# Kernel optimization log

Measured on AMD Instinct MI355X. Metric: run time of the kernel, lower is better.

Reference implementation:

```python
import jax, jax.numpy as jnp
import numpy as np

DIM = 768
HEADS = 12
HEAD_DIM = DIM // HEADS
EPS = 1e-5


def layernorm(x, gamma, beta):
    mu = jnp.mean(x, axis=-1, keepdims=True)
    var = jnp.var(x, axis=-1, keepdims=True)
    return (x - mu) * jax.lax.rsqrt(var + EPS) * gamma + beta


def setup_inputs() -> dict:
    key = jax.random.key(0)
    ks = jax.random.split(key, 9)
    B, N, C = 4, 2048, DIM
    s_in = 1.0 / np.sqrt(C)
    return {
        "x": jax.random.normal(ks[0], (B, N, C), dtype=jnp.float32),
        "qkv_w": jax.random.normal(ks[1], (3 * C, C), dtype=jnp.float32) * s_in,
        "qkv_b": jnp.zeros((3 * C,), dtype=jnp.float32),
        "proj_w": jax.random.normal(ks[2], (C, C), dtype=jnp.float32) * s_in,
        "proj_b": jnp.zeros((C,), dtype=jnp.float32),
        "q_gamma": jnp.ones((HEAD_DIM,), dtype=jnp.float32),
        "q_beta": jnp.zeros((HEAD_DIM,), dtype=jnp.float32),
        "k_gamma": jnp.ones((HEAD_DIM,), dtype=jnp.float32),
        "k_beta": jnp.zeros((HEAD_DIM,), dtype=jnp.float32),
    }


def reference(x, qkv_w, qkv_b, proj_w, proj_b, q_gamma, q_beta, k_gamma, k_beta):
    B, N, C = x.shape
    H, Dh = HEADS, C // HEADS
    scale = Dh ** (-0.5)
    # qkv projection: [B,N,3C] -> [3,B,H,N,Dh]
    qkv = (x @ qkv_w.T + qkv_b).reshape(B, N, 3, H, Dh).transpose(2, 0, 3, 1, 4)
    q, k, v = qkv[0], qkv[1], qkv[2]
    q = layernorm(q, q_gamma, q_beta)
    k = layernorm(k, k_gamma, k_beta)
    # explicit full score matrix [B,H,N,N] as in the original module
    attn = jnp.einsum("bhqd,bhkd->bhqk", q, k) * scale
    attn = jax.nn.softmax(attn, axis=-1)
    out = jnp.einsum("bhqk,bhkd->bhqd", attn, v)  # [B,H,N,Dh]
    out = out.transpose(0, 2, 1, 3).reshape(B, N, C)
    return out @ proj_w.T + proj_b
```

## Files before the change

### kernel.cpp

```cpp
#include <hip/hip_runtime.h>
#include <hip/hip_bf16.h>
#include <cstdint>
#include <cstddef>

#define BB 4
#define SEQ 2048
#define CD 768
#define NH 12
#define DH 64
#define MROWS (BB*SEQ)
#define NQKV (3*CD)

typedef float f32x4 __attribute__((ext_vector_type(4)));
typedef float f32x16 __attribute__((ext_vector_type(16)));
typedef short bf16x8 __attribute__((ext_vector_type(8)));

static __device__ __forceinline__ unsigned short f2bf(float f) {
  union { float f; unsigned int u; } cv; cv.f = f;
  unsigned int u = cv.u;
  unsigned int r = (u + 0x7FFFu + ((u >> 16) & 1u)) >> 16;
  return (unsigned short)r;
}

static __device__ __forceinline__ float fexp2(float x) {
#if __has_builtin(__builtin_amdgcn_exp2f)
  return __builtin_amdgcn_exp2f(x);
#else
  float r; asm("v_exp_f32 %0, %1" : "=v"(r) : "v"(x)); return r;
#endif
}

#define GAS __attribute__((address_space(1)))
#define LAS __attribute__((address_space(3)))
static __device__ __forceinline__ void gl2lds16(const void* g, void* l) {
  __builtin_amdgcn_global_load_lds((const GAS void*)g, (LAS void*)l, 16, 0, 0);
}

#define MFMA(a, b, c) __builtin_amdgcn_mfma_f32_16x16x32_bf16((a), (b), (c), 0, 0, 0)
#define MFMA32(a, b, c) __builtin_amdgcn_mfma_f32_32x32x16_bf16((a), (b), (c), 0, 0, 0)
#define PACKBF(dst, x, y) asm("v_cvt_pk_bf16_f32 %0, %1, %2" : "=v"(dst) : "v"(x), "v"(y))
#define SWAP32(a, b) asm("v_permlane32_swap_b32 %0, %1" : "+v"(a), "+v"(b))

#define QSC 0.18033688011112042f

__global__ __launch_bounds__(256) void cvt_bf16(const float* __restrict__ in,
                                                unsigned short* __restrict__ out, int n4) {
  int i = blockIdx.x * 256 + threadIdx.x;
  if (i >= n4) return;
  float4 v = reinterpret_cast<const float4*>(in)[i];
  unsigned int lo = (unsigned int)f2bf(v.x) | ((unsigned int)f2bf(v.y) << 16);
  unsigned int hi = (unsigned int)f2bf(v.z) | ((unsigned int)f2bf(v.w) << 16);
  reinterpret_cast<uint2*>(out)[i] = make_uint2(lo, hi);
}

__global__ __launch_bounds__(256) void qkv_gemm(
    const unsigned short* __restrict__ Xb, const unsigned short* __restrict__ Wb,
    const float* __restrict__ bias,
    const float* __restrict__ qg, const float* __restrict__ qbt,
    const float* __restrict__ kg, const float* __restrict__ kbt,
    unsigned short* __restrict__ Qo, unsigned short* __restrict__ Ko,
    unsigned short* __restrict__ Vt) {
  __shared__ unsigned short Als[2][128 * 64];
  __shared__ unsigned short Bls[2][128 * 64];
  const int tid = threadIdx.x;
  const int wid = tid >> 6, lane = tid & 63;
  const int g = lane >> 4, cl = lane & 15;
  const int wr = (wid >> 1) * 64, wc = (wid & 1) * 64;

  const int wg = blockIdx.x;
  const int wgid = (wg & 7) * 144 + (wg >> 3);
  const int bm = wgid / 18, bn = wgid % 18;

  f32x4 acc[4][4] = {};

  const int srow = tid >> 3;
  const int scol = ((tid & 7) ^ (srow & 7)) * 8;
  const unsigned short* Abase = Xb + (size_t)(bm * 128 + srow) * CD + scol;
  const unsigned short* Bbase = Wb + (size_t)(bn * 128 + srow) * CD + scol;

#define QSTG(buf, kt)                                                         \
  do {                                                                        \
    gl2lds16(Abase + (size_t)0 * 32 * CD + (kt) * 64, &Als[buf][0 * 2048 + tid * 8]); \
    gl2lds16(Abase + (size_t)1 * 32 * CD + (kt) * 64, &Als[buf][1 * 2048 + tid * 8]); \
    gl2lds16(Abase + (size_t)2 * 32 * CD + (kt) * 64, &Als[buf][2 * 2048 + tid * 8]); \
    gl2lds16(Abase + (size_t)3 * 32 * CD + (kt) * 64, &Als[buf][3 * 2048 + tid * 8]); \
    gl2lds16(Bbase + (size_t)0 * 32 * CD + (kt) * 64, &Bls[buf][0 * 2048 + tid * 8]); \
    gl2lds16(Bbase + (size_t)1 * 32 * CD + (kt) * 64, &Bls[buf][1 * 2048 + tid * 8]); \
    gl2lds16(Bbase + (size_t)2 * 32 * CD + (kt) * 64, &Bls[buf][2 * 2048 + tid * 8]); \
    gl2lds16(Bbase + (size_t)3 * 32 * CD + (kt) * 64, &Bls[buf][3 * 2048 + tid * 8]); \
  } while (0)

  QSTG(0, 0);
  __syncthreads();
  const int NKT = CD / 64;
  for (int kt = 0; kt < NKT; ++kt) {
    const int cur = kt & 1;
    if (kt + 1 < NKT) QSTG(cur ^ 1, kt + 1);
    bf16x8 bfr[4][2];
#pragma unroll
    for (int j = 0; j < 4; ++j) {
      const int Bcol = wc + j * 16 + cl;
      const int sw = (Bcol & 7) << 3;
      bfr[j][0] = *(const bf16x8*)&Bls[cur][Bcol * 64 + ((g * 8) ^ sw)];
      bfr[j][1] = *(const bf16x8*)&Bls[cur][Bcol * 64 + ((32 + g * 8) ^ sw)];
    }
    __builtin_amdgcn_s_setprio(1);
#pragma unroll
    for (int i = 0; i < 4; ++i) {
      const int Arow = wr + i * 16 + cl;
      const int sw = (Arow & 7) << 3;
      bf16x8 a0 = *(const bf16x8*)&Als[cur][Arow * 64 + ((g * 8) ^ sw)];
      bf16x8 a1 = *(const bf16x8*)&Als[cur][Arow * 64 + ((32 + g * 8) ^ sw)];
#pragma unroll
      for (int j = 0; j < 4; ++j) {
        acc[i][j] = MFMA(a0, bfr[j][0], acc[i][j]);
        acc[i][j] = MFMA(a1, bfr[j][1], acc[i][j]);
      }
    }
    __builtin_amdgcn_s_setprio(0);
    __syncthreads();
  }
#undef QSTG

  const int j0 = bn * 128 + wc;
  const int t = j0 / CD;
  const int h = (j0 % CD) / DH;
  float bia[4], gam[4] = {0, 0, 0, 0}, bet[4] = {0, 0, 0, 0};
#pragma unroll
  for (int j = 0; j < 4; ++j) {
    int d = j * 16 + cl;
    bia[j] = bias[j0 + d];
    if (t == 0) { gam[j] = qg[d] * QSC; bet[j] = qbt[d] * QSC; }
    else if (t == 1) { gam[j] = kg[d]; bet[j] = kbt[d]; }
  }

  if (t == 2) {
#pragma unroll
    for (int i = 0; i < 4; ++i) {
      const int mrow = bm * 128 + wr + i * 16 + g * 4;
      const int b = mrow >> 11, nn = mrow & 2047;
#pragma unroll
      for (int j = 0; j < 4; ++j) {
        const int d = j * 16 + cl;
        unsigned int lo = (unsigned int)f2bf(acc[i][j][0] + bia[j]) |
                          ((unsigned int)f2bf(acc[i][j][1] + bia[j]) << 16);
        unsigned int hi2 = (unsigned int)f2bf(acc[i][j][2] + bia[j]) |
                           ((unsigned int)f2bf(acc[i][j][3] + bia[j]) << 16);
        *reinterpret_cast<uint2*>(&Vt[((size_t)(b * NH + h) * DH + d) * SEQ + nn]) =
            make_uint2(lo, hi2);
      }
    }
    return;
  }

  unsigned short* Out = (t == 0) ? Qo : Ko;
#pragma unroll
  for (int i = 0; i < 4; ++i) {
#pragma unroll
    for (int r = 0; r < 4; ++r) {
      float vj[4];
#pragma unroll
      for (int j = 0; j < 4; ++j) vj[j] = acc[i][j][r] + bia[j];
      const int m = bm * 128 + wr + i * 16 + g * 4 + r;
      const int b = m >> 11, n = m & 2047;
      size_t base = ((size_t)(b * NH + h) * SEQ + n) * DH;
      float s = vj[0] + vj[1] + vj[2] + vj[3];
      float ss = vj[0] * vj[0] + vj[1] * vj[1] + vj[2] * vj[2] + vj[3] * vj[3];
#pragma unroll
      for (int msk = 1; msk < 16; msk <<= 1) {
        s += __shfl_xor(s, msk, 64);
        ss += __shfl_xor(ss, msk, 64);
      }
      float mu = s * (1.0f / 64.0f);
      float var = ss * (1.0f / 64.0f) - mu * mu;
      float rstd = rsqrtf(var + 1e-5f);
#pragma unroll
      for (int j = 0; j < 4; ++j)
        Out[base + j * 16 + cl] = f2bf((vj[j] - mu) * rstd * gam[j] + bet[j]);
    }
  }
}

__global__ __launch_bounds__(256, 3) void attn_fwd(
    const unsigned short* __restrict__ Qb, const unsigned short* __restrict__ Kb,
    const unsigned short* __restrict__ Vtb, unsigned short* __restrict__ Ob) {
  __shared__ unsigned short kl[2][64 * 64];
  __shared__ unsigned short vt[2][64 * 64];
  const int tid = threadIdx.x, wave = tid >> 6, lane = tid & 63;
  const int q32 = lane & 31, hi = lane >> 5;

  const int wg = blockIdx.x;
  const int lin = (wg & 7) * 96 + (wg >> 3);
  const int bh = lin >> 4;
  const int qbase = (lin & 15) * 128 + wave * 32;

  const unsigned short* qrow = Qb + ((size_t)bh * SEQ + qbase + q32) * DH + hi * 8;
  bf16x8 qf[4];
#pragma unroll
  for (int dc = 0; dc < 4; ++dc) qf[dc] = *(const bf16x8*)&qrow[dc * 16];

  const unsigned short* Kh = Kb + (size_t)bh * SEQ * DH;
  const unsigned short* Vth = Vtb + (size_t)bh * DH * SEQ;

  const int sr = tid >> 3;
  const int sc = 8 * ((tid & 7) ^ (sr & 7));
  const int ksw = (q32 & 7) << 3;

  const short oneb = (short)0x3F80;
  const bf16x8 onesv = {oneb, oneb, oneb, oneb, oneb, oneb, oneb, oneb};

#define ASTAGE(buf, kb0)                                                      \
  do {                                                                        \
    gl2lds16(&Kh[(size_t)((kb0) + sr) * DH + sc], &kl[buf][tid * 8]);         \
    gl2lds16(&Kh[(size_t)((kb0) + sr + 32) * DH + sc], &kl[buf][tid * 8 + 2048]); \
    gl2lds16(&Vth[(size_t)sr * SEQ + (kb0) + sc], &vt[buf][tid * 8]);         \
    gl2lds16(&Vth[(size_t)(sr + 32) * SEQ + (kb0) + sc], &vt[buf][tid * 8 + 2048]); \
  } while (0)

  f32x16 o0 = {}, o1 = {}, ol = {};

  ASTAGE(0, 0);
  __syncthreads();
  const int NT = SEQ / 64;
#pragma unroll 2
  for (int it = 0; it < NT; ++it) {
    const int cur = it & 1;
    if (it + 1 < NT) ASTAGE(cur ^ 1, (it + 1) * 64);

    f32x16 s0 = {}, s1 = {};
    __builtin_amdgcn_s_setprio(1);
#pragma unroll
    for (int dc = 0; dc < 4; ++dc) {
      const int colb = dc * 16 + hi * 8;
      bf16x8 kf0 = *(const bf16x8*)&kl[cur][q32 * 64 + (colb ^ ksw)];
      bf16x8 kf1 = *(const bf16x8*)&kl[cur][(32 + q32) * 64 + (colb ^ ksw)];
      s0 = MFMA32(kf0, qf[dc], s0);
      s1 = MFMA32(kf1, qf[dc], s1);
    }
    __builtin_amdgcn_s_setprio(0);

#pragma unroll
    for (int r = 0; r < 16; ++r) {
      s0[r] = fexp2(s0[r]);
      s1[r] = fexp2(s1[r]);
    }

    bf16x8 pav[4];
#pragma unroll
    for (int c = 0; c < 4; ++c) {
      const int b = 8 * (c & 1);
      unsigned int wA0, wA1, wB0, wB1;
      if (c < 2) {
        PACKBF(wA0, s0[b + 0], s0[b + 1]); PACKBF(wA1, s0[b + 2], s0[b + 3]);
        PACKBF(wB0, s0[b + 4], s0[b + 5]); PACKBF(wB1, s0[b + 6], s0[b + 7]);
      } else {
        PACKBF(wA0, s1[b + 0], s1[b + 1]); PACKBF(wA1, s1[b + 2], s1[b + 3]);
        PACKBF(wB0, s1[b + 4], s1[b + 5]); PACKBF(wB1, s1[b + 6], s1[b + 7]);
      }
      SWAP32(wA0, wB0);
      SWAP32(wA1, wB1);
      union { unsigned int w[4]; bf16x8 v; } u;
      u.w[0] = wA0; u.w[1] = wA1; u.w[2] = wB0; u.w[3] = wB1;
      pav[c] = u.v;
    }

    __builtin_amdgcn_s_setprio(1);
#pragma unroll
    for (int c = 0; c < 4; ++c) {
      const int colb = c * 16 + hi * 8;
      bf16x8 vf0 = *(const bf16x8*)&vt[cur][q32 * 64 + (colb ^ ksw)];
      bf16x8 vf1 = *(const bf16x8*)&vt[cur][(32 + q32) * 64 + (colb ^ ksw)];
      o0 = MFMA32(pav[c], vf0, o0);
      o1 = MFMA32(pav[c], vf1, o1);
      ol = MFMA32(pav[c], onesv, ol);
    }
    __builtin_amdgcn_s_setprio(0);
    __syncthreads();
  }
#undef ASTAGE

  const int b = bh / NH, h = bh % NH;
#pragma unroll
  for (int r = 0; r < 16; ++r) {
    const int qq = (r & 3) + 8 * (r >> 2) + 4 * hi;
    const float iv = __builtin_amdgcn_rcpf(ol[r]);
    size_t base = ((size_t)(b * SEQ + qbase + qq)) * CD + h * DH;
    Ob[base + q32] = f2bf(o0[r] * iv);
    Ob[base + 32 + q32] = f2bf(o1[r] * iv);
  }
}

__global__ __launch_bounds__(256) void proj_gemm(
    const unsigned short* __restrict__ Ab, const unsigned short* __restrict__ Wb,
    const float* __restrict__ bias, float* __restrict__ out) {
  __shared__ unsigned short Als[2][128 * 64];
  __shared__ unsigned short Bls[2][128 * 64];
  const int tid = threadIdx.x;
  const int wid = tid >> 6, lane = tid & 63;
  const int g = lane >> 4, cl = lane & 15;
  const int bm = blockIdx.x, bn = blockIdx.y;
  const int wr = (wid >> 1) * 64, wc = (wid & 1) * 64;

  f32x4 acc[4][4] = {};

  const int srow = tid >> 3;
  const int scol = ((tid & 7) ^ (srow & 7)) * 8;
  const unsigned short* Abase = Ab + (size_t)(bm * 128 + srow) * CD + scol;
  const unsigned short* Bbase = Wb + (size_t)(bn * 128 + srow) * CD + scol;

#define PSTG(buf, kt)                                                         \
  do {                                                                        \
    gl2lds16(Abase + (size_t)0 * 32 * CD + (kt) * 64, &Als[buf][0 * 2048 + tid * 8]); \
    gl2lds16(Abase + (size_t)1 * 32 * CD + (kt) * 64, &Als[buf][1 * 2048 + tid * 8]); \
    gl2lds16(Abase + (size_t)2 * 32 * CD + (kt) * 64, &Als[buf][2 * 2048 + tid * 8]); \
    gl2lds16(Abase + (size_t)3 * 32 * CD + (kt) * 64, &Als[buf][3 * 2048 + tid * 8]); \
    gl2lds16(Bbase + (size_t)0 * 32 * CD + (kt) * 64, &Bls[buf][0 * 2048 + tid * 8]); \
    gl2lds16(Bbase + (size_t)1 * 32 * CD + (kt) * 64, &Bls[buf][1 * 2048 + tid * 8]); \
    gl2lds16(Bbase + (size_t)2 * 32 * CD + (kt) * 64, &Bls[buf][2 * 2048 + tid * 8]); \
    gl2lds16(Bbase + (size_t)3 * 32 * CD + (kt) * 64, &Bls[buf][3 * 2048 + tid * 8]); \
  } while (0)

  PSTG(0, 0);
  __syncthreads();
  const int NKT = CD / 64;
  for (int kt = 0; kt < NKT; ++kt) {
    const int cur = kt & 1;
    if (kt + 1 < NKT) PSTG(cur ^ 1, kt + 1);
    bf16x8 bfr[4][2];
#pragma unroll
    for (int j = 0; j < 4; ++j) {
      const int Bcol = wc + j * 16 + cl;
      const int sw = (Bcol & 7) << 3;
      bfr[j][0] = *(const bf16x8*)&Bls[cur][Bcol * 64 + ((g * 8) ^ sw)];
      bfr[j][1] = *(const bf16x8*)&Bls[cur][Bcol * 64 + ((32 + g * 8) ^ sw)];
    }
    __builtin_amdgcn_s_setprio(1);
#pragma unroll
    for (int i = 0; i < 4; ++i) {
      const int Arow = wr + i * 16 + cl;
      const int sw = (Arow & 7) << 3;
      bf16x8 a0 = *(const bf16x8*)&Als[cur][Arow * 64 + ((g * 8) ^ sw)];
      bf16x8 a1 = *(const bf16x8*)&Als[cur][Arow * 64 + ((32 + g * 8) ^ sw)];
#pragma unroll
      for (int j = 0; j < 4; ++j) {
        acc[i][j] = MFMA(a0, bfr[j][0], acc[i][j]);
        acc[i][j] = MFMA(a1, bfr[j][1], acc[i][j]);
      }
    }
    __builtin_amdgcn_s_setprio(0);
    __syncthreads();
  }
#undef PSTG

  const int j0 = bn * 128 + wc;
  float pb4[4];
#pragma unroll
  for (int j = 0; j < 4; ++j) pb4[j] = bias[j0 + j * 16 + cl];
#pragma unroll
  for (int i = 0; i < 4; ++i) {
#pragma unroll
    for (int r = 0; r < 4; ++r) {
      const int m = bm * 128 + wr + i * 16 + g * 4 + r;
      float* orow = out + (size_t)m * CD + j0;
#pragma unroll
      for (int j = 0; j < 4; ++j) orow[j * 16 + cl] = acc[i][j][r] + pb4[j];
    }
  }
}

extern "C" void kernel_launch(void* const* d_in, const int* in_sizes, int n_in,
                              void* d_out, int out_size, void* d_ws, size_t ws_size,
                              hipStream_t stream) {
  const float* x = (const float*)d_in[0];
  const float* qkv_w = (const float*)d_in[1];
  const float* qkv_b = (const float*)d_in[2];
  const float* proj_w = (const float*)d_in[3];
  const float* proj_b = (const float*)d_in[4];
  const float* q_gamma = (const float*)d_in[5];
  const float* q_beta = (const float*)d_in[6];
  const float* k_gamma = (const float*)d_in[7];
  const float* k_beta = (const float*)d_in[8];
  float* out = (float*)d_out;

  char* w = (char*)d_ws;
  unsigned short* Xb = (unsigned short*)w; w += (size_t)MROWS * CD * 2;
  unsigned short* Wq = (unsigned short*)w; w += (size_t)NQKV * CD * 2;
  unsigned short* Wp = (unsigned short*)w; w += (size_t)CD * CD * 2;
  unsigned short* Qo = (unsigned short*)w; w += (size_t)BB * NH * SEQ * DH * 2;
  unsigned short* Ko = (unsigned short*)w; w += (size_t)BB * NH * SEQ * DH * 2;
  unsigned short* Vt = (unsigned short*)w; w += (size_t)BB * NH * SEQ * DH * 2;
  unsigned short* Ob = (unsigned short*)w; w += (size_t)MROWS * CD * 2;

  cvt_bf16<<<MROWS * CD / 1024, 256, 0, stream>>>(x, Xb, MROWS * CD / 4);
  cvt_bf16<<<NQKV * CD / 1024, 256, 0, stream>>>(qkv_w, Wq, NQKV * CD / 4);
  cvt_bf16<<<CD * CD / 1024, 256, 0, stream>>>(proj_w, Wp, CD * CD / 4);

  qkv_gemm<<<(MROWS / 128) * (NQKV / 128), 256, 0, stream>>>(
      Xb, Wq, qkv_b, q_gamma, q_beta, k_gamma, k_beta, Qo, Ko, Vt);

  attn_fwd<<<SEQ / 128 * BB * NH, 256, 0, stream>>>(Qo, Ko, Vt, Ob);

  proj_gemm<<<dim3(MROWS / 128, CD / 128), 256, 0, stream>>>(Ob, Wp, proj_b, out);
}
```

Before: 147.8 us.

## Split attention key tiles across wave pairs and reduce partials through LDS

Each attention block now covers 64 queries instead of 128. Two wave pairs split every 64-key tile in half, and their partial outputs and denominators are summed through shared memory at the end. This doubles the grid and cuts per-wave score registers, with the launch bound raised to 4 blocks per CU to improve occupancy. The cost is that K/V tiles are loaded twice as often per query, plus an extra LDS reduction and barrier. The ones-MFMA for the row sum still runs, now over half as many keys per wave.

```diff
diff --git a/kernel.cpp b/kernel.cpp
--- a/kernel.cpp
+++ b/kernel.cpp
@@ -181,18 +181,19 @@
   }
 }
 
-__global__ __launch_bounds__(256, 3) void attn_fwd(
+__global__ __launch_bounds__(256, 4) void attn_fwd(
     const unsigned short* __restrict__ Qb, const unsigned short* __restrict__ Kb,
     const unsigned short* __restrict__ Vtb, unsigned short* __restrict__ Ob) {
   __shared__ unsigned short kl[2][64 * 64];
   __shared__ unsigned short vt[2][64 * 64];
   const int tid = threadIdx.x, wave = tid >> 6, lane = tid & 63;
   const int q32 = lane & 31, hi = lane >> 5;
+  const int qg = wave & 1, kh = wave >> 1;
 
   const int wg = blockIdx.x;
-  const int lin = (wg & 7) * 96 + (wg >> 3);
-  const int bh = lin >> 4;
-  const int qbase = (lin & 15) * 128 + wave * 32;
+  const int lin = (wg & 7) * 192 + (wg >> 3);
+  const int bh = lin >> 5;
+  const int qbase = (lin & 31) * 64 + qg * 32;
 
   const unsigned short* qrow = Qb + ((size_t)bh * SEQ + qbase + q32) * DH + hi * 8;
   bf16x8 qf[4];
@@ -205,6 +206,7 @@
   const int sr = tid >> 3;
   const int sc = 8 * ((tid & 7) ^ (sr & 7));
   const int ksw = (q32 & 7) << 3;
+  const int krow = kh * 32 + q32;
 
   const short oneb = (short)0x3F80;
   const bf16x8 onesv = {oneb, oneb, oneb, oneb, oneb, oneb, oneb, oneb};
@@ -227,36 +229,25 @@
     const int cur = it & 1;
     if (it + 1 < NT) ASTAGE(cur ^ 1, (it + 1) * 64);
 
-    f32x16 s0 = {}, s1 = {};
+    f32x16 s = {};
     __builtin_amdgcn_s_setprio(1);
 #pragma unroll
     for (int dc = 0; dc < 4; ++dc) {
-      const int colb = dc * 16 + hi * 8;
-      bf16x8 kf0 = *(const bf16x8*)&kl[cur][q32 * 64 + (colb ^ ksw)];
-      bf16x8 kf1 = *(const bf16x8*)&kl[cur][(32 + q32) * 64 + (colb ^ ksw)];
-      s0 = MFMA32(kf0, qf[dc], s0);
-      s1 = MFMA32(kf1, qf[dc], s1);
+      bf16x8 kf = *(const bf16x8*)&kl[cur][krow * 64 + ((dc * 16 + hi * 8) ^ ksw)];
+      s = MFMA32(kf, qf[dc], s);
     }
     __builtin_amdgcn_s_setprio(0);
 
 #pragma unroll
-    for (int r = 0; r < 16; ++r) {
-      s0[r] = fexp2(s0[r]);
-      s1[r] = fexp2(s1[r]);
-    }
-
-    bf16x8 pav[4];
-#pragma unroll
-    for (int c = 0; c < 4; ++c) {
-      const int b = 8 * (c & 1);
+    for (int r = 0; r < 16; ++r) s[r] = fexp2(s[r]);
+
+    bf16x8 pav[2];
+#pragma unroll
+    for (int c = 0; c < 2; ++c) {
+      const int b = 8 * c;
       unsigned int wA0, wA1, wB0, wB1;
-      if (c < 2) {
-        PACKBF(wA0, s0[b + 0], s0[b + 1]); PACKBF(wA1, s0[b + 2], s0[b + 3]);
-        PACKBF(wB0, s0[b + 4], s0[b + 5]); PACKBF(wB1, s0[b + 6], s0[b + 7]);
-      } else {
-        PACKBF(wA0, s1[b + 0], s1[b + 1]); PACKBF(wA1, s1[b + 2], s1[b + 3]);
-        PACKBF(wB0, s1[b + 4], s1[b + 5]); PACKBF(wB1, s1[b + 6], s1[b + 7]);
-      }
+      PACKBF(wA0, s[b + 0], s[b + 1]); PACKBF(wA1, s[b + 2], s[b + 3]);
+      PACKBF(wB0, s[b + 4], s[b + 5]); PACKBF(wB1, s[b + 6], s[b + 7]);
       SWAP32(wA0, wB0);
       SWAP32(wA1, wB1);
       union { unsigned int w[4]; bf16x8 v; } u;
@@ -266,8 +257,8 @@
 
     __builtin_amdgcn_s_setprio(1);
 #pragma unroll
-    for (int c = 0; c < 4; ++c) {
-      const int colb = c * 16 + hi * 8;
+    for (int c = 0; c < 2; ++c) {
+      const int colb = kh * 32 + c * 16 + hi * 8;
       bf16x8 vf0 = *(const bf16x8*)&vt[cur][q32 * 64 + (colb ^ ksw)];
       bf16x8 vf1 = *(const bf16x8*)&vt[cur][(32 + q32) * 64 + (colb ^ ksw)];
       o0 = MFMA32(pav[c], vf0, o0);
@@ -279,14 +270,29 @@
   }
 #undef ASTAGE
 
-  const int b = bh / NH, h = bh % NH;
-#pragma unroll
-  for (int r = 0; r < 16; ++r) {
-    const int qq = (r & 3) + 8 * (r >> 2) + 4 * hi;
-    const float iv = __builtin_amdgcn_rcpf(ol[r]);
-    size_t base = ((size_t)(b * SEQ + qbase + qq)) * CD + h * DH;
-    Ob[base + q32] = f2bf(o0[r] * iv);
-    Ob[base + 32 + q32] = f2bf(o1[r] * iv);
+  float* fb = qg ? (float*)&vt[0][0] : (float*)&kl[0][0];
+  if (kh == 1) {
+#pragma unroll
+    for (int r = 0; r < 16; ++r) {
+      fb[r * 64 + lane] = o0[r];
+      fb[1024 + r * 64 + lane] = o1[r];
+      fb[2048 + r * 64 + lane] = ol[r];
+    }
+  }
+  __syncthreads();
+  if (kh == 0) {
+    const int b = bh / NH, h = bh % NH;
+#pragma unroll
+    for (int r = 0; r < 16; ++r) {
+      const float p0 = o0[r] + fb[r * 64 + lane];
+      const float p1 = o1[r] + fb[1024 + r * 64 + lane];
+      const float pl = ol[r] + fb[2048 + r * 64 + lane];
+      const int qq = (r & 3) + 8 * (r >> 2) + 4 * hi;
+      const float iv = __builtin_amdgcn_rcpf(pl);
+      size_t base = ((size_t)(b * SEQ + qbase + qq)) * CD + h * DH;
+      Ob[base + q32] = f2bf(p0 * iv);
+      Ob[base + 32 + q32] = f2bf(p1 * iv);
+    }
   }
 }
 
@@ -398,7 +404,7 @@
   qkv_gemm<<<(MROWS / 128) * (NQKV / 128), 256, 0, stream>>>(
       Xb, Wq, qkv_b, q_gamma, q_beta, k_gamma, k_beta, Qo, Ko, Vt);
 
-  attn_fwd<<<SEQ / 128 * BB * NH, 256, 0, stream>>>(Qo, Ko, Vt, Ob);
+  attn_fwd<<<(SEQ / 64) * BB * NH, 256, 0, stream>>>(Qo, Ko, Vt, Ob);
 
   proj_gemm<<<dim3(MROWS / 128, CD / 128), 256, 0, stream>>>(Ob, Wp, proj_b, out);
 }
```

Result: slower. 157.8 us (+6.8%).
